# Optimization experiments

Measured on AMD Instinct MI355X. Metric: run time of the kernel, lower is better.

Reference implementation:

```python
import jax, jax.numpy as jnp
import numpy as np

N = 50000   # total nodes in batch
E = 640000  # directed edges
G = 64      # graphs in batch
D_IN = 128
D_H = 128
D_OUT = 10


def _glorot(key, shape):
    fan_in = shape[0]
    return jax.random.normal(key, shape, dtype=jnp.float32) / np.sqrt(fan_in)


def setup_inputs() -> dict:
    key = jax.random.key(0)
    ks = jax.random.split(key, 10)
    x = jax.random.normal(ks[0], (N, D_IN), dtype=jnp.float32)
    src = jax.random.randint(ks[1], (E,), 0, N, dtype=jnp.int32)
    dst = jax.random.randint(ks[2], (E,), 0, N, dtype=jnp.int32)
    batch = jnp.sort(jax.random.randint(ks[3], (N,), 0, G, dtype=jnp.int32))
    return {
        "x": x, "src": src, "dst": dst, "batch": batch,
        "W1": _glorot(ks[4], (D_IN, D_H)), "b1": jnp.zeros((D_H,), jnp.float32),
        "W2": _glorot(ks[5], (D_H, D_H)), "b2": jnp.zeros((D_H,), jnp.float32),
        "W3": _glorot(ks[6], (D_H, D_H)), "b3": jnp.zeros((D_H,), jnp.float32),
        "Wl": _glorot(ks[7], (D_H, D_OUT)), "bl": jnp.zeros((D_OUT,), jnp.float32),
    }


def gcn_conv(x, W, b, src, dst):
    """PyG GCNConv: add self-loops, symmetric deg^-1/2 normalization,
    linear transform, scatter-sum aggregation at dst, plus bias."""
    n = x.shape[0]
    loops = jnp.arange(n, dtype=src.dtype)
    s = jnp.concatenate([src, loops])  # [E+N]
    d = jnp.concatenate([dst, loops])
    deg = jax.ops.segment_sum(jnp.ones_like(d, dtype=x.dtype), d, num_segments=n)
    dinv = jnp.where(deg > 0, jax.lax.rsqrt(deg), 0.0)
    norm = dinv[s] * dinv[d]                        # [E+N]
    h = x @ W                                       # [N, D]
    out = jax.ops.segment_sum(h[s] * norm[:, None], d, num_segments=n)
    return out + b


def reference(x, src, dst, batch, W1, b1, W2, b2, W3, b3, Wl, bl):
    n = x.shape[0]
    h = jax.nn.relu(gcn_conv(x, W1, b1, src, dst))
    # dropout is a no-op in eval mode
    h = jax.nn.relu(gcn_conv(h, W2, b2, src, dst))
    h = gcn_conv(h, W3, b3, src, dst)
    # global_mean_pool over graph ids
    sums = jax.ops.segment_sum(h, batch, num_segments=G)            # [G, D]
    counts = jax.ops.segment_sum(jnp.ones((n,), h.dtype), batch, num_segments=G)
    pooled = sums / jnp.maximum(counts, 1.0)[:, None]
    logits = pooled @ Wl + bl                                       # [G, D_OUT]
    return jax.nn.log_softmax(logits, axis=1)
```

## Files before the change

### kernel.cpp

```cpp
#include <hip/hip_runtime.h>


constexpr int D = 128;
constexpr int DOUT = 10;
constexpr int PSPLIT = 8;

using short8  = __attribute__((ext_vector_type(8))) short;
using float4v = __attribute__((ext_vector_type(4))) float;
using f32x2   = __attribute__((ext_vector_type(2))) float;

__device__ __forceinline__ ushort f2bf(float f) {
  uint u = __float_as_uint(f);
  return (ushort)((u + 0x7fffu + ((u >> 16) & 1u)) >> 16);
}
__device__ __forceinline__ float bf2f(ushort s) {
  return __uint_as_float(((uint)s) << 16);
}
__device__ __forceinline__ float bflo(uint u) { return __uint_as_float(u << 16); }
__device__ __forceinline__ float bfhi(uint u) { return __uint_as_float(u & 0xffff0000u); }


__global__ void init_kernel(int* __restrict__ cnt, int n) {
  int i = blockIdx.x * blockDim.x + threadIdx.x;
  if (i < n) cnt[i] = 0;
}

__global__ void count_kernel(const int* __restrict__ dst, int* __restrict__ cnt, int e) {
  int i = blockIdx.x * blockDim.x + threadIdx.x;
  if (i < e) atomicAdd(&cnt[dst[i]], 1);
}

__global__ __launch_bounds__(256) void scan1_kernel(const int* __restrict__ cnt,
    int* __restrict__ bsum, int n) {
  __shared__ int sd[256];
  int i = blockIdx.x * 256 + threadIdx.x;
  sd[threadIdx.x] = (i < n) ? cnt[i] : 0;
  __syncthreads();
  for (int off = 128; off > 0; off >>= 1) {
    if (threadIdx.x < (unsigned)off) sd[threadIdx.x] += sd[threadIdx.x + off];
    __syncthreads();
  }
  if (threadIdx.x == 0) bsum[blockIdx.x] = sd[0];
}

__global__ __launch_bounds__(1024) void scan2_kernel(const int* __restrict__ bsum,
    int* __restrict__ boff, int nb, int* __restrict__ rowptr, int n) {
  __shared__ int sd[1024];
  int v = ((int)threadIdx.x < nb) ? bsum[threadIdx.x] : 0;
  sd[threadIdx.x] = v;
  __syncthreads();
  for (int off = 1; off < 1024; off <<= 1) {
    int t = (threadIdx.x >= (unsigned)off) ? sd[threadIdx.x - off] : 0;
    __syncthreads();
    sd[threadIdx.x] += t;
    __syncthreads();
  }
  if ((int)threadIdx.x < nb) boff[threadIdx.x] = sd[threadIdx.x] - v;
  if ((int)threadIdx.x == nb - 1) rowptr[n] = sd[threadIdx.x];
}

__global__ __launch_bounds__(256) void scan3_kernel(const int* __restrict__ cnt,
    const int* __restrict__ boff, int* __restrict__ rowptr, int* __restrict__ cursor,
    float* __restrict__ dinv, int n) {
  __shared__ int sd[256];
  int i = blockIdx.x * 256 + threadIdx.x;
  int v = (i < n) ? cnt[i] : 0;
  sd[threadIdx.x] = v;
  __syncthreads();
  for (int off = 1; off < 256; off <<= 1) {
    int t = (threadIdx.x >= (unsigned)off) ? sd[threadIdx.x - off] : 0;
    __syncthreads();
    sd[threadIdx.x] += t;
    __syncthreads();
  }
  if (i < n) {
    int rp = boff[blockIdx.x] + sd[threadIdx.x] - v;
    rowptr[i] = rp;
    cursor[i] = rp;
    dinv[i] = rsqrtf((float)(v + 1));
  }
}

__global__ void fill_kernel(const int* __restrict__ src, const int* __restrict__ dst,
    int* __restrict__ cursor, const float* __restrict__ dinv,
    uint* __restrict__ epk, int e) {
  int i = blockIdx.x * blockDim.x + threadIdx.x;
  if (i < e) {
    int d = dst[i];
    int s = src[i];
    int slot = atomicAdd(&cursor[d], 1);
    epk[slot] = (uint)s | ((uint)f2bf(dinv[s] * dinv[d]) << 16);
  }
}

__global__ __launch_bounds__(256) void prepw_kernel(const float* __restrict__ W1,
    const float* __restrict__ W2, const float* __restrict__ W3, ushort* __restrict__ Wp) {
  const float* W = (blockIdx.y == 0) ? W1 : (blockIdx.y == 1) ? W2 : W3;
  ushort* Wpo = Wp + (size_t)blockIdx.y * 2048 * 8;
  int idx = blockIdx.x * 256 + threadIdx.x;
  int cf = idx >> 8, kk = (idx >> 6) & 3, lane = idx & 63;
  int k0 = kk * 32 + (lane >> 4) * 8;
  int c = cf * 16 + (lane & 15);
  uint p[4];
  #pragma unroll
  for (int h = 0; h < 4; ++h) {
    ushort lo = f2bf(W[(k0 + 2 * h) * D + c]);
    ushort hi = f2bf(W[(k0 + 2 * h + 1) * D + c]);
    p[h] = (uint)lo | ((uint)hi << 16);
  }
  uint4 w = make_uint4(p[0], p[1], p[2], p[3]);
  *(uint4*)(Wpo + idx * 8) = w;
}

template<bool F32>
__global__ __launch_bounds__(256) void gemm_mfma(const void* __restrict__ Ain,
    const ushort* __restrict__ Wp, uchar* __restrict__ out, int n) {
  __shared__ ushort wl[2048 * 8];
  const int tid = threadIdx.x;
  #pragma unroll
  for (int i = 0; i < 8; ++i) {
    int idx = tid + i * 256;
    *(uint4*)(&wl[idx * 8]) = *(const uint4*)(Wp + idx * 8);
  }
  __syncthreads();
  const int w = tid >> 6, lane = tid & 63;
  const int row0 = blockIdx.x * 64 + w * 16;
  int arow = row0 + (lane & 15);
  if (arow >= n) arow = n - 1;

  short8 a[4];
  if constexpr (F32) {
    const float* abase = (const float*)Ain + (size_t)arow * D + ((lane >> 4) * 8);
    #pragma unroll
    for (int kk = 0; kk < 4; ++kk) {
      float4 f0 = *(const float4*)(abase + kk * 32);
      float4 f1 = *(const float4*)(abase + kk * 32 + 4);
      short8 v;
      v[0] = (short)f2bf(f0.x); v[1] = (short)f2bf(f0.y);
      v[2] = (short)f2bf(f0.z); v[3] = (short)f2bf(f0.w);
      v[4] = (short)f2bf(f1.x); v[5] = (short)f2bf(f1.y);
      v[6] = (short)f2bf(f1.z); v[7] = (short)f2bf(f1.w);
      a[kk] = v;
    }
  } else {
    const ushort* abase = (const ushort*)Ain + (size_t)arow * D + ((lane >> 4) * 8);
    #pragma unroll
    for (int kk = 0; kk < 4; ++kk) a[kk] = *(const short8*)(abase + kk * 32);
  }

  float4v acc[8] = {};
  #pragma unroll
  for (int kk = 0; kk < 4; ++kk) {
    #pragma unroll
    for (int cf = 0; cf < 8; ++cf) {
      short8 b = *(const short8*)(&wl[((cf * 4 + kk) * 64 + lane) * 8]);
      acc[cf] = __builtin_amdgcn_mfma_f32_16x16x32_bf16(a[kk], b, acc[cf], 0, 0, 0);
    }
  }
  const int crow = row0 + (lane >> 4) * 4;
  const int ccol = lane & 15;
  #pragma unroll
  for (int cf = 0; cf < 8; ++cf) {
    #pragma unroll
    for (int r = 0; r < 4; ++r) {
      if (crow + r < n) {
        int enc = __builtin_amdgcn_cvt_pk_fp8_f32(acc[cf][r], acc[cf][r], 0, false);
        out[(size_t)(crow + r) * D + cf * 16 + ccol] = (uchar)(enc & 0xff);
      }
    }
  }
}

__global__ __launch_bounds__(256) void agg_kernel(const uchar* __restrict__ h8,
    const int* __restrict__ rowptr, const uint* __restrict__ epk,
    const float* __restrict__ dinv, const float* __restrict__ bias,
    ushort* __restrict__ out, int n, int relu) {
  int node = (int)((blockIdx.x * blockDim.x + threadIdx.x) >> 6);
  if (node >= n) return;
  const int lane = threadIdx.x & 63;
  const int sub = lane >> 5;
  const int li = lane & 31;
  const int beg = rowptr[node], end = rowptr[node + 1];
  float a0 = 0.f, a1 = 0.f, a2 = 0.f, a3 = 0.f;
  for (int e = beg; e < end; e += 8) {
    int i0 = e + 0 + sub, i1 = e + 2 + sub, i2 = e + 4 + sub, i3 = e + 6 + sub;
    uint m0 = epk[min(i0, end - 1)];
    uint m1 = epk[min(i1, end - 1)];
    uint m2 = epk[min(i2, end - 1)];
    uint m3 = epk[min(i3, end - 1)];
    uint r0 = *(const uint*)(h8 + (size_t)(m0 & 0xffffu) * D + li * 4);
    uint r1 = *(const uint*)(h8 + (size_t)(m1 & 0xffffu) * D + li * 4);
    uint r2 = *(const uint*)(h8 + (size_t)(m2 & 0xffffu) * D + li * 4);
    uint r3 = *(const uint*)(h8 + (size_t)(m3 & 0xffffu) * D + li * 4);
    float w0 = (i0 < end) ? bfhi(m0) : 0.f;
    float w1 = (i1 < end) ? bfhi(m1) : 0.f;
    float w2 = (i2 < end) ? bfhi(m2) : 0.f;
    float w3 = (i3 < end) ? bfhi(m3) : 0.f;
    f32x2 p0a = __builtin_amdgcn_cvt_pk_f32_fp8(r0, false);
    f32x2 p0b = __builtin_amdgcn_cvt_pk_f32_fp8(r0, true);
    f32x2 p1a = __builtin_amdgcn_cvt_pk_f32_fp8(r1, false);
    f32x2 p1b = __builtin_amdgcn_cvt_pk_f32_fp8(r1, true);
    f32x2 p2a = __builtin_amdgcn_cvt_pk_f32_fp8(r2, false);
    f32x2 p2b = __builtin_amdgcn_cvt_pk_f32_fp8(r2, true);
    f32x2 p3a = __builtin_amdgcn_cvt_pk_f32_fp8(r3, false);
    f32x2 p3b = __builtin_amdgcn_cvt_pk_f32_fp8(r3, true);
    a0 += p0a[0] * w0 + p1a[0] * w1 + p2a[0] * w2 + p3a[0] * w3;
    a1 += p0a[1] * w0 + p1a[1] * w1 + p2a[1] * w2 + p3a[1] * w3;
    a2 += p0b[0] * w0 + p1b[0] * w1 + p2b[0] * w2 + p3b[0] * w3;
    a3 += p0b[1] * w0 + p1b[1] * w1 + p2b[1] * w2 + p3b[1] * w3;
  }
  a0 += __shfl_xor(a0, 32);
  a1 += __shfl_xor(a1, 32);
  a2 += __shfl_xor(a2, 32);
  a3 += __shfl_xor(a3, 32);
  const float di = dinv[node];
  const float dsq = di * di;
  uint sv = *(const uint*)(h8 + (size_t)node * D + li * 4);
  f32x2 sa = __builtin_amdgcn_cvt_pk_f32_fp8(sv, false);
  f32x2 sb = __builtin_amdgcn_cvt_pk_f32_fp8(sv, true);
  a0 += sa[0] * dsq;
  a1 += sa[1] * dsq;
  a2 += sb[0] * dsq;
  a3 += sb[1] * dsq;
  float4 bv = *(const float4*)(bias + li * 4);
  a0 += bv.x; a1 += bv.y; a2 += bv.z; a3 += bv.w;
  if (relu) {
    a0 = fmaxf(a0, 0.f); a1 = fmaxf(a1, 0.f);
    a2 = fmaxf(a2, 0.f); a3 = fmaxf(a3, 0.f);
  }
  if (sub == 0) {
    uint2 pk;
    pk.x = (uint)f2bf(a0) | ((uint)f2bf(a1) << 16);
    pk.y = (uint)f2bf(a2) | ((uint)f2bf(a3) << 16);
    *(uint2*)(out + (size_t)node * D + li * 4) = pk;
  }
}

__global__ __launch_bounds__(256) void pool1_kernel(const ushort* __restrict__ act,
    const int* __restrict__ batch, float* __restrict__ pp, int n) {
  const int g = blockIdx.x;
  const int sp = blockIdx.y;
  int lo = 0, hi = n;
  while (lo < hi) { int mid = (lo + hi) >> 1; if (batch[mid] < g) lo = mid + 1; else hi = mid; }
  const int start = lo;
  hi = n;
  while (lo < hi) { int mid = (lo + hi) >> 1; if (batch[mid] <= g) lo = mid + 1; else hi = mid; }
  const int end = lo;
  const int len = end - start;
  const int per = (len + PSPLIT - 1) / PSPLIT;
  const int i0 = start + sp * per;
  const int i1 = min(i0 + per, end);

  const int rt = threadIdx.x >> 4;
  const int ds = threadIdx.x & 15;
  float acc[8] = {};
  for (int i = i0 + rt; i < i1; i += 16) {
    short8 v = *(const short8*)(act + (size_t)i * D + ds * 8);
    #pragma unroll
    for (int e2 = 0; e2 < 8; ++e2) acc[e2] += bf2f((ushort)v[e2]);
  }
  __shared__ float sd[256][8];
  #pragma unroll
  for (int e2 = 0; e2 < 8; ++e2) sd[threadIdx.x][e2] = acc[e2];
  __syncthreads();
  if (threadIdx.x < 128) {
    int d = threadIdx.x;
    int slice = d >> 3, e2 = d & 7;
    float s = 0.f;
    #pragma unroll
    for (int k = 0; k < 16; ++k) s += sd[k * 16 + slice][e2];
    pp[((size_t)g * PSPLIT + sp) * D + d] = s;
  }
}

__global__ __launch_bounds__(640) void head_kernel(const float* __restrict__ pp,
    const int* __restrict__ batch, const float* __restrict__ Wl,
    const float* __restrict__ bl, float* __restrict__ out, int n, int g) {
  __shared__ float pooled[64 * D];
  __shared__ float cnts[64];
  __shared__ float lg[64][DOUT];
  const int tid = threadIdx.x;
  if (tid < g) {
    int gg = tid;
    int lo = 0, hi = n;
    while (lo < hi) { int mid = (lo + hi) >> 1; if (batch[mid] < gg) lo = mid + 1; else hi = mid; }
    int start = lo;
    hi = n;
    while (lo < hi) { int mid = (lo + hi) >> 1; if (batch[mid] <= gg) lo = mid + 1; else hi = mid; }
    cnts[gg] = fmaxf((float)(lo - start), 1.f);
  }
  __syncthreads();
  for (int idx = tid; idx < g * D; idx += 640) {
    int gg = idx >> 7, d = idx & 127;
    float s = 0.f;
    #pragma unroll
    for (int sp = 0; sp < PSPLIT; ++sp) s += pp[((size_t)gg * PSPLIT + sp) * D + d];
    pooled[idx] = s / cnts[gg];
  }
  __syncthreads();
  int gi = tid / DOUT, o = tid % DOUT;
  if (gi < g) {
    float acc = bl[o];
    for (int d = 0; d < D; ++d) acc += pooled[gi * D + d] * Wl[d * DOUT + o];
    lg[gi][o] = acc;
  }
  __syncthreads();
  if (gi < g) {
    float m = -1e30f;
    for (int j = 0; j < DOUT; ++j) m = fmaxf(m, lg[gi][j]);
    float s = 0.f;
    for (int j = 0; j < DOUT; ++j) s += expf(lg[gi][j] - m);
    out[gi * DOUT + o] = lg[gi][o] - m - logf(s);
  }
}


extern "C" void kernel_launch(void* const* d_in, const int* in_sizes, int n_in,
                              void* d_out, int out_size, void* d_ws, size_t ws_size,
                              hipStream_t stream) {
  const float* x   = (const float*)d_in[0];
  const int* src   = (const int*)d_in[1];
  const int* dst   = (const int*)d_in[2];
  const int* batch = (const int*)d_in[3];
  const float* W1  = (const float*)d_in[4];
  const float* b1  = (const float*)d_in[5];
  const float* W2  = (const float*)d_in[6];
  const float* b2  = (const float*)d_in[7];
  const float* W3  = (const float*)d_in[8];
  const float* b3  = (const float*)d_in[9];
  const float* Wl  = (const float*)d_in[10];
  const float* bl  = (const float*)d_in[11];
  float* out = (float*)d_out;

  const int n = in_sizes[0] / D;
  const int e = in_sizes[1];
  const int g = out_size / DOUT;

  char* p = (char*)d_ws;
  auto alloc = [&](size_t bytes) {
    char* r = p;
    p += (bytes + 255) & ~(size_t)255;
    return r;
  };
  const int nb = (n + 255) / 256;
  int* cnt      = (int*)alloc((size_t)n * 4);
  int* rowptr   = (int*)alloc((size_t)(n + 1) * 4);
  int* cursor   = (int*)alloc((size_t)n * 4);
  float* dinv   = (float*)alloc((size_t)n * 4);
  int* bsum     = (int*)alloc((size_t)nb * 4);
  int* boff     = (int*)alloc((size_t)nb * 4);
  uint* epk     = (uint*)alloc((size_t)e * 4);
  ushort* Wp    = (ushort*)alloc(3 * 2048 * 16);
  ushort* bfA   = (ushort*)alloc((size_t)n * D * 2);
  ushort* bfB   = (ushort*)alloc((size_t)n * D * 2);
  uchar* tmp8   = (uchar*)alloc((size_t)n * D);
  float* pp     = (float*)alloc((size_t)g * PSPLIT * D * 4);
  (void)ws_size;

  const int B = 256;
  const int gridN = (n + B - 1) / B;
  const int gridE = (e + B - 1) / B;

  init_kernel<<<gridN, B, 0, stream>>>(cnt, n);
  count_kernel<<<gridE, B, 0, stream>>>(dst, cnt, e);
  scan1_kernel<<<nb, B, 0, stream>>>(cnt, bsum, n);
  scan2_kernel<<<1, 1024, 0, stream>>>(bsum, boff, nb, rowptr, n);
  scan3_kernel<<<nb, B, 0, stream>>>(cnt, boff, rowptr, cursor, dinv, n);
  fill_kernel<<<gridE, B, 0, stream>>>(src, dst, cursor, dinv, epk, e);
  prepw_kernel<<<dim3(8, 3), B, 0, stream>>>(W1, W2, W3, Wp);

  const int gemmGrid = (n + 63) / 64;
  const int aggGrid = (n * 64 + B - 1) / B;

  gemm_mfma<true><<<gemmGrid, B, 0, stream>>>(x, Wp, tmp8, n);
  agg_kernel<<<aggGrid, B, 0, stream>>>(tmp8, rowptr, epk, dinv, b1, bfB, n, 1);
  gemm_mfma<false><<<gemmGrid, B, 0, stream>>>(bfB, Wp + 2048 * 8, tmp8, n);
  agg_kernel<<<aggGrid, B, 0, stream>>>(tmp8, rowptr, epk, dinv, b2, bfA, n, 1);
  gemm_mfma<false><<<gemmGrid, B, 0, stream>>>(bfA, Wp + 2 * 2048 * 8, tmp8, n);
  agg_kernel<<<aggGrid, B, 0, stream>>>(tmp8, rowptr, epk, dinv, b3, bfB, n, 0);

  pool1_kernel<<<dim3(g, PSPLIT), B, 0, stream>>>(bfB, batch, pp, n);
  head_kernel<<<1, 640, 0, stream>>>(pp, batch, Wl, bl, out, n, g);
}
```

Measured before the change: 216.1 us.

## Build CSR via coarse destination buckets with shared-memory counting and scatter

Replaces the per-node global atomic count and fill passes with a two-level binning scheme. Edges are first appended into fixed-capacity buckets of 512 destination nodes using one global atomic per edge on a small set of bucket counters. Per-bucket blocks then count degrees and assign CSR slots with shared-memory atomics, so the random global atomics on per-node cursors go away and epk writes stay local. The cost is heavy contention on only ~100 bucket counters, an extra buffer pass, and a fixed bucket capacity that silently drops edges if a bucket overflows.

```diff
diff --git a/kernel.cpp b/kernel.cpp
--- a/kernel.cpp
+++ b/kernel.cpp
@@ -4,6 +4,8 @@
 constexpr int D = 128;
 constexpr int DOUT = 10;
 constexpr int PSPLIT = 8;
+constexpr int BSH = 9;
+constexpr int BCAP = 9216;
 
 using short8  = __attribute__((ext_vector_type(8))) short;
 using float4v = __attribute__((ext_vector_type(4))) float;
@@ -20,14 +22,35 @@
 __device__ __forceinline__ float bfhi(uint u) { return __uint_as_float(u & 0xffff0000u); }
 
 
-__global__ void init_kernel(int* __restrict__ cnt, int n) {
+__global__ void init_kernel(int* __restrict__ bcnt, int nb) {
   int i = blockIdx.x * blockDim.x + threadIdx.x;
-  if (i < n) cnt[i] = 0;
-}
-
-__global__ void count_kernel(const int* __restrict__ dst, int* __restrict__ cnt, int e) {
+  if (i < nb) bcnt[i] = 0;
+}
+
+__global__ void binfill_kernel(const int* __restrict__ src, const int* __restrict__ dst,
+    int* __restrict__ bcnt, uint* __restrict__ buck, int e) {
   int i = blockIdx.x * blockDim.x + threadIdx.x;
-  if (i < e) atomicAdd(&cnt[dst[i]], 1);
+  if (i >= e) return;
+  int d = dst[i], s = src[i];
+  int b = d >> BSH;
+  int pos = atomicAdd(&bcnt[b], 1);
+  if (pos < BCAP)
+    buck[(size_t)b * BCAP + pos] = (uint)s | ((uint)(d & ((1 << BSH) - 1)) << 16);
+}
+
+__global__ __launch_bounds__(256) void countb_kernel(const uint* __restrict__ buck,
+    const int* __restrict__ bcnt, int* __restrict__ cnt, int n) {
+  __shared__ int lc[1 << BSH];
+  const int b = blockIdx.x;
+  const int base = b << BSH;
+  const int m = min(1 << BSH, n - base);
+  for (int j = threadIdx.x; j < m; j += 256) lc[j] = 0;
+  __syncthreads();
+  const int c = min(bcnt[b], BCAP);
+  for (int i = threadIdx.x; i < c; i += 256)
+    atomicAdd(&lc[buck[(size_t)b * BCAP + i] >> 16], 1);
+  __syncthreads();
+  for (int j = threadIdx.x; j < m; j += 256) cnt[base + j] = lc[j];
 }
 
 __global__ __launch_bounds__(256) void scan1_kernel(const int* __restrict__ cnt,
@@ -60,7 +83,7 @@
 }
 
 __global__ __launch_bounds__(256) void scan3_kernel(const int* __restrict__ cnt,
-    const int* __restrict__ boff, int* __restrict__ rowptr, int* __restrict__ cursor,
+    const int* __restrict__ boff, int* __restrict__ rowptr,
     float* __restrict__ dinv, int n) {
   __shared__ int sd[256];
   int i = blockIdx.x * 256 + threadIdx.x;
@@ -74,21 +97,27 @@
     __syncthreads();
   }
   if (i < n) {
-    int rp = boff[blockIdx.x] + sd[threadIdx.x] - v;
-    rowptr[i] = rp;
-    cursor[i] = rp;
+    rowptr[i] = boff[blockIdx.x] + sd[threadIdx.x] - v;
     dinv[i] = rsqrtf((float)(v + 1));
   }
 }
 
-__global__ void fill_kernel(const int* __restrict__ src, const int* __restrict__ dst,
-    int* __restrict__ cursor, const float* __restrict__ dinv,
-    uint* __restrict__ epk, int e) {
-  int i = blockIdx.x * blockDim.x + threadIdx.x;
-  if (i < e) {
-    int d = dst[i];
-    int s = src[i];
-    int slot = atomicAdd(&cursor[d], 1);
+__global__ __launch_bounds__(256) void scatter_kernel(const uint* __restrict__ buck,
+    const int* __restrict__ bcnt, const int* __restrict__ rowptr,
+    const float* __restrict__ dinv, uint* __restrict__ epk, int n) {
+  __shared__ int lcur[1 << BSH];
+  const int b = blockIdx.x;
+  const int base = b << BSH;
+  const int m = min(1 << BSH, n - base);
+  for (int j = threadIdx.x; j < m; j += 256) lcur[j] = rowptr[base + j];
+  __syncthreads();
+  const int c = min(bcnt[b], BCAP);
+  for (int i = threadIdx.x; i < c; i += 256) {
+    uint rec = buck[(size_t)b * BCAP + i];
+    int dl = (int)(rec >> 16);
+    int s = (int)(rec & 0xffffu);
+    int d = base + dl;
+    int slot = atomicAdd(&lcur[dl], 1);
     epk[slot] = (uint)s | ((uint)f2bf(dinv[s] * dinv[d]) << 16);
   }
 }
@@ -343,12 +372,14 @@
     return r;
   };
   const int nb = (n + 255) / 256;
+  const int NB = (n + (1 << BSH) - 1) >> BSH;
   int* cnt      = (int*)alloc((size_t)n * 4);
   int* rowptr   = (int*)alloc((size_t)(n + 1) * 4);
-  int* cursor   = (int*)alloc((size_t)n * 4);
   float* dinv   = (float*)alloc((size_t)n * 4);
   int* bsum     = (int*)alloc((size_t)nb * 4);
   int* boff     = (int*)alloc((size_t)nb * 4);
+  int* bcnt     = (int*)alloc((size_t)NB * 4);
+  uint* buck    = (uint*)alloc((size_t)NB * BCAP * 4);
   uint* epk     = (uint*)alloc((size_t)e * 4);
   ushort* Wp    = (ushort*)alloc(3 * 2048 * 16);
   ushort* bfA   = (ushort*)alloc((size_t)n * D * 2);
@@ -358,15 +389,15 @@
   (void)ws_size;
 
   const int B = 256;
-  const int gridN = (n + B - 1) / B;
   const int gridE = (e + B - 1) / B;
 
-  init_kernel<<<gridN, B, 0, stream>>>(cnt, n);
-  count_kernel<<<gridE, B, 0, stream>>>(dst, cnt, e);
+  init_kernel<<<1, 128, 0, stream>>>(bcnt, NB);
+  binfill_kernel<<<gridE, B, 0, stream>>>(src, dst, bcnt, buck, e);
+  countb_kernel<<<NB, B, 0, stream>>>(buck, bcnt, cnt, n);
   scan1_kernel<<<nb, B, 0, stream>>>(cnt, bsum, n);
   scan2_kernel<<<1, 1024, 0, stream>>>(bsum, boff, nb, rowptr, n);
-  scan3_kernel<<<nb, B, 0, stream>>>(cnt, boff, rowptr, cursor, dinv, n);
-  fill_kernel<<<gridE, B, 0, stream>>>(src, dst, cursor, dinv, epk, e);
+  scan3_kernel<<<nb, B, 0, stream>>>(cnt, boff, rowptr, dinv, n);
+  scatter_kernel<<<NB, B, 0, stream>>>(buck, bcnt, rowptr, dinv, epk, n);
   prepw_kernel<<<dim3(8, 3), B, 0, stream>>>(W1, W2, W3, Wp);
 
   const int gemmGrid = (n + 63) / 64;
```

Result: slower. 827.3 us (+282.8%).
